# Optimization experiments

Measured on AMD Instinct MI355X. Metric: run time of the kernel, lower is better.

Reference implementation:

```python
import jax, jax.numpy as jnp
import numpy as np

NODES = 14      # input_size: nodes per graph
IN_F = 24       # seq_len: node feature dim
HID1 = 32
HID2 = 64       # hid_feats
HEADS = 2
OUT = 24        # output_size
B = 2048        # number of graphs
SLOPE = 0.2


def _make_edges():
    # fully connected (no self loops) within each 14-node graph
    pairs = np.array([(i, j) for i in range(NODES) for j in range(NODES) if i != j]).T  # [2,182]
    offs = (np.arange(B) * NODES)[:, None]
    src = (pairs[0][None, :] + offs).reshape(-1)
    dst = (pairs[1][None, :] + offs).reshape(-1)
    return np.stack([src, dst]).astype(np.int32)  # [2, 372736]


def setup_inputs() -> dict:
    key = jax.random.key(0)
    ks = jax.random.split(key, 16)
    N = B * NODES
    x = jax.random.normal(ks[0], (N, IN_F), dtype=jnp.float32)
    y = jax.random.normal(ks[1], (N, OUT), dtype=jnp.float32)
    edge_index = jnp.asarray(_make_edges())
    batch = jnp.repeat(jnp.arange(B, dtype=jnp.int32), NODES)
    s = 0.1
    params = dict(
        W1=jax.random.normal(ks[2], (IN_F, HEADS * HID1), dtype=jnp.float32) * s,
        a_src1=jax.random.normal(ks[3], (HEADS, HID1), dtype=jnp.float32) * s,
        a_dst1=jax.random.normal(ks[4], (HEADS, HID1), dtype=jnp.float32) * s,
        b1=jnp.zeros((HID1,), dtype=jnp.float32),
        W2=jax.random.normal(ks[5], (HID1, HEADS * HID2), dtype=jnp.float32) * s,
        a_src2=jax.random.normal(ks[6], (HEADS, HID2), dtype=jnp.float32) * s,
        a_dst2=jax.random.normal(ks[7], (HEADS, HID2), dtype=jnp.float32) * s,
        b2=jnp.zeros((HID2,), dtype=jnp.float32),
        Wf1=jax.random.normal(ks[8], (NODES, HID2, 8), dtype=jnp.float32) * s,
        bf1=jnp.zeros((NODES, 8), dtype=jnp.float32),
        Wf2=jax.random.normal(ks[9], (NODES, 8, OUT), dtype=jnp.float32) * s,
        bf2=jnp.zeros((NODES, OUT), dtype=jnp.float32),
    )
    return {"x": x, "y": y, "edge_index": edge_index, "batch": batch, **params}


def gat_conv(x, src, dst, W, a_src, a_dst, b):
    # PyG GATConv, concat=False (mean over heads), self-loops already in src/dst
    N = x.shape[0]
    H, F = a_src.shape
    xh = (x @ W).reshape(N, H, F)                       # [N,H,F]
    al_s = (xh * a_src).sum(-1)                         # [N,H]
    al_d = (xh * a_dst).sum(-1)                         # [N,H]
    alpha = jax.nn.leaky_relu(al_s[src] + al_d[dst], SLOPE)  # [E,H]
    amax = jax.ops.segment_max(alpha, dst, num_segments=N)
    ex = jnp.exp(alpha - amax[dst])
    den = jax.ops.segment_sum(ex, dst, num_segments=N)
    w = ex / den[dst]                                   # softmax per target node
    out = jax.ops.segment_sum(w[:, :, None] * xh[src], dst, num_segments=N)  # [N,H,F]
    return out.mean(axis=1) + b


def reference(x, y, edge_index, batch, W1, a_src1, a_dst1, b1, W2, a_src2, a_dst2, b2, Wf1, bf1, Wf2, bf2):
    N = x.shape[0]
    loops = jnp.arange(N, dtype=edge_index.dtype)
    src = jnp.concatenate([edge_index[0], loops])
    dst = jnp.concatenate([edge_index[1], loops])
    h = jax.nn.elu(gat_conv(x, src, dst, W1, a_src1, a_dst1, b1))   # [N,32]
    h = gat_conv(h, src, dst, W2, a_src2, a_dst2, b2)               # [N,64]
    # batch regroup: batch ids are contiguous per graph, so the Python
    # gather-loop in the original is exactly a reshape
    nb = N // NODES
    xg = h.reshape(nb, NODES, HID2).transpose(1, 0, 2)   # [14, B, 64]
    yg = y.reshape(nb, NODES, OUT)                       # [B, 14, out]
    # per-node-index MLP ensemble, batched over the 14 indices
    hh = jax.nn.relu(jnp.einsum('kbh,kho->kbo', xg, Wf1) + bf1[:, None, :])
    pred = jax.nn.sigmoid(jnp.einsum('kbo,kop->kbp', hh, Wf2) + bf2[:, None, :])  # [14,B,out]
    return pred, yg
```

## Files before the change

kernel.cpp:

```cpp
#include <hip/hip_runtime.h>

#define NODES 14
#define IN_F 24
#define HID1 32
#define HID2 64
#define OUT_F 24
#define SLOPE 0.2f

#define U_US1 0
#define U_UD1 48
#define U_US2 96
#define U_UD2 160

#define GPB 4
#define PHASE_FENCE() __builtin_amdgcn_sched_barrier(0)

__global__ __launch_bounds__(256) void compute_uvecs(
    const float* __restrict__ W1, const float* __restrict__ a_src1,
    const float* __restrict__ a_dst1,
    const float* __restrict__ W2, const float* __restrict__ a_src2,
    const float* __restrict__ a_dst2, float* __restrict__ u)
{
  const int tid = threadIdx.x;
  if (tid < 96) {
    const int sd = (tid >= 48), r = tid - sd * 48;
    const int h = (r >= IN_F), k = r - h * IN_F;
    const float* av = sd ? a_dst1 : a_src1;
    float s = 0.f;
#pragma unroll
    for (int f = 0; f < HID1; ++f)
      s += W1[k * 64 + h * HID1 + f] * av[h * HID1 + f];
    u[(sd ? U_UD1 : U_US1) + h * IN_F + k] = s;
  } else if (tid < 224) {
    const int j = tid - 96;
    const int sd = (j >= 64), r = j - sd * 64;
    const int h = (r >= HID1), k = r - h * HID1;
    const float* av = sd ? a_dst2 : a_src2;
    float s = 0.f;
#pragma unroll
    for (int f = 0; f < HID2; ++f)
      s += W2[k * 128 + h * HID2 + f] * av[h * HID2 + f];
    u[(sd ? U_UD2 : U_US2) + h * HID1 + k] = s;
  }
}

__global__ __launch_bounds__(64 * GPB) void gnn_fused(
    const float* __restrict__ x, const float* __restrict__ y,
    const float* __restrict__ W1, const float* __restrict__ b1,
    const float* __restrict__ W2, const float* __restrict__ b2,
    const float* __restrict__ Wf1, const float* __restrict__ bf1,
    const float* __restrict__ Wf2, const float* __restrict__ bf2,
    const float* __restrict__ uvec,
    float* __restrict__ out, int ngraphs)
{
  const int tid  = threadIdx.x;
  const int lane = tid & 63;
  const int wv   = tid >> 6;
  const int gu   = __builtin_amdgcn_readfirstlane(blockIdx.x * GPB + wv);
  if (gu >= ngraphs) return;

  __shared__ __align__(16) float h1s[GPB][NODES * 32];
  __shared__ __align__(16) float h2s[GPB][NODES * 64];
  __shared__ __align__(16) float wt[GPB][28 * 16];
  __shared__ __align__(16) float als[GPB][32];
  __shared__ __align__(16) float ald[GPB][32];
  __shared__ __align__(16) float hhs[GPB][112];

  const float* xg = x + (size_t)gu * (NODES * IN_F);

  {
    const float4* y4 = (const float4*)(y + (size_t)gu * (NODES * OUT_F));
    float4* o4 = (float4*)(out + (size_t)NODES * ngraphs * OUT_F
                               + (size_t)gu * (NODES * OUT_F));
    for (int i = lane; i < (NODES * OUT_F) / 4; i += 64) o4[i] = y4[i];
  }

  float xcol[NODES];
  {
    float w1r[IN_F];
#pragma unroll
    for (int k = 0; k < IN_F; ++k) w1r[k] = W1[k * 64 + lane];
#pragma unroll 2
    for (int n = 0; n < NODES; ++n) {
      float acc = 0.f;
#pragma unroll
      for (int k = 0; k < IN_F; ++k) acc += xg[n * IN_F + k] * w1r[k];
      xcol[n] = acc;
    }
  }
  PHASE_FENCE();

  if (lane < 56) {
    const int n = lane >> 2, h = (lane >> 1) & 1, sd = lane & 1;
    const float* uu = uvec + (sd ? U_UD1 : U_US1) + h * IN_F;
    float s = 0.f;
#pragma unroll
    for (int k4 = 0; k4 < 6; ++k4) {
      const float4 xv = *(const float4*)&xg[n * IN_F + k4 * 4];
      const float4 uv = *(const float4*)&uu[k4 * 4];
      s += xv.x * uv.x + xv.y * uv.y + xv.z * uv.z + xv.w * uv.w;
    }
    (sd ? ald : als)[wv][h * 16 + n] = s;
  }
  if (lane < NODES * 2) {
    const int j = lane >> 1, h = lane & 1;
    const float ad = ald[wv][h * 16 + j];
    const float4 A0 = *(const float4*)&als[wv][h * 16 + 0];
    const float4 A1 = *(const float4*)&als[wv][h * 16 + 4];
    const float4 A2 = *(const float4*)&als[wv][h * 16 + 8];
    const float2 A3 = *(const float2*)&als[wv][h * 16 + 12];
    float a[NODES] = {A0.x, A0.y, A0.z, A0.w, A1.x, A1.y, A1.z, A1.w,
                      A2.x, A2.y, A2.z, A2.w, A3.x, A3.y};
    float m = -1e30f;
#pragma unroll
    for (int i = 0; i < NODES; ++i) {
      float v = a[i] + ad;
      v = v > 0.f ? v : SLOPE * v;
      a[i] = v; m = fmaxf(m, v);
    }
    float den = 0.f;
#pragma unroll
    for (int i = 0; i < NODES; ++i) { a[i] = __expf(a[i] - m); den += a[i]; }
    const float r = 1.f / den;
    float* wr = &wt[wv][(j * 2 + h) * 16];
    *(float4*)&wr[0]  = make_float4(a[0]*r,  a[1]*r,  a[2]*r,  a[3]*r);
    *(float4*)&wr[4]  = make_float4(a[4]*r,  a[5]*r,  a[6]*r,  a[7]*r);
    *(float4*)&wr[8]  = make_float4(a[8]*r,  a[9]*r,  a[10]*r, a[11]*r);
    *(float2*)&wr[12] = make_float2(a[12]*r, a[13]*r);
  }
  PHASE_FENCE();

  {
    const int h = lane >> 5, f5 = lane & 31;
    const float bb = b1[f5];
#pragma unroll 2
    for (int n = 0; n < NODES; ++n) {
      const float* wr = &wt[wv][(n * 2 + h) * 16];
      const float4 w0 = *(const float4*)&wr[0];
      const float4 w1 = *(const float4*)&wr[4];
      const float4 w2 = *(const float4*)&wr[8];
      const float2 w3 = *(const float2*)&wr[12];
      float o = w0.x*xcol[0] + w0.y*xcol[1] + w0.z*xcol[2] + w0.w*xcol[3]
              + w1.x*xcol[4] + w1.y*xcol[5] + w1.z*xcol[6] + w1.w*xcol[7]
              + w2.x*xcol[8] + w2.y*xcol[9] + w2.z*xcol[10] + w2.w*xcol[11]
              + w3.x*xcol[12] + w3.y*xcol[13];
      const float oo = __shfl_xor(o, 32);
      if (h == 0) {
        const float v = 0.5f * (o + oo) + bb;
        h1s[wv][n * 32 + f5] = v > 0.f ? v : expm1f(v);
      }
    }
  }
  PHASE_FENCE();

  float acc0[NODES], acc1[NODES];
#pragma unroll
  for (int n = 0; n < NODES; ++n) { acc0[n] = 0.f; acc1[n] = 0.f; }
#pragma unroll
  for (int c = 0; c < 2; ++c) {
    float w2a[16], w2b[16];
#pragma unroll
    for (int j = 0; j < 16; ++j) {
      w2a[j] = W2[(c * 16 + j) * 128 + lane];
      w2b[j] = W2[(c * 16 + j) * 128 + 64 + lane];
    }
#pragma unroll 2
    for (int n = 0; n < NODES; ++n) {
      const float4 v0 = *(const float4*)&h1s[wv][n * 32 + c * 16 + 0];
      const float4 v1 = *(const float4*)&h1s[wv][n * 32 + c * 16 + 4];
      const float4 v2 = *(const float4*)&h1s[wv][n * 32 + c * 16 + 8];
      const float4 v3 = *(const float4*)&h1s[wv][n * 32 + c * 16 + 12];
      acc0[n] += v0.x*w2a[0] + v0.y*w2a[1] + v0.z*w2a[2] + v0.w*w2a[3]
               + v1.x*w2a[4] + v1.y*w2a[5] + v1.z*w2a[6] + v1.w*w2a[7]
               + v2.x*w2a[8] + v2.y*w2a[9] + v2.z*w2a[10] + v2.w*w2a[11]
               + v3.x*w2a[12] + v3.y*w2a[13] + v3.z*w2a[14] + v3.w*w2a[15];
      acc1[n] += v0.x*w2b[0] + v0.y*w2b[1] + v0.z*w2b[2] + v0.w*w2b[3]
               + v1.x*w2b[4] + v1.y*w2b[5] + v1.z*w2b[6] + v1.w*w2b[7]
               + v2.x*w2b[8] + v2.y*w2b[9] + v2.z*w2b[10] + v2.w*w2b[11]
               + v3.x*w2b[12] + v3.y*w2b[13] + v3.z*w2b[14] + v3.w*w2b[15];
    }
    PHASE_FENCE();
  }

  if (lane < 56) {
    const int n = lane >> 2, h = (lane >> 1) & 1, sd = lane & 1;
    const float* uu = uvec + (sd ? U_UD2 : U_US2) + h * HID1;
    float s = 0.f;
#pragma unroll
    for (int k4 = 0; k4 < 8; ++k4) {
      const float4 hv = *(const float4*)&h1s[wv][n * 32 + k4 * 4];
      const float4 uv = *(const float4*)&uu[k4 * 4];
      s += hv.x * uv.x + hv.y * uv.y + hv.z * uv.z + hv.w * uv.w;
    }
    (sd ? ald : als)[wv][h * 16 + n] = s;
  }
  if (lane < NODES * 2) {
    const int j = lane >> 1, h = lane & 1;
    const float ad = ald[wv][h * 16 + j];
    const float4 A0 = *(const float4*)&als[wv][h * 16 + 0];
    const float4 A1 = *(const float4*)&als[wv][h * 16 + 4];
    const float4 A2 = *(const float4*)&als[wv][h * 16 + 8];
    const float2 A3 = *(const float2*)&als[wv][h * 16 + 12];
    float a[NODES] = {A0.x, A0.y, A0.z, A0.w, A1.x, A1.y, A1.z, A1.w,
                      A2.x, A2.y, A2.z, A2.w, A3.x, A3.y};
    float m = -1e30f;
#pragma unroll
    for (int i = 0; i < NODES; ++i) {
      float v = a[i] + ad;
      v = v > 0.f ? v : SLOPE * v;
      a[i] = v; m = fmaxf(m, v);
    }
    float den = 0.f;
#pragma unroll
    for (int i = 0; i < NODES; ++i) { a[i] = __expf(a[i] - m); den += a[i]; }
    const float r = 1.f / den;
    float* wr = &wt[wv][(j * 2 + h) * 16];
    *(float4*)&wr[0]  = make_float4(a[0]*r,  a[1]*r,  a[2]*r,  a[3]*r);
    *(float4*)&wr[4]  = make_float4(a[4]*r,  a[5]*r,  a[6]*r,  a[7]*r);
    *(float4*)&wr[8]  = make_float4(a[8]*r,  a[9]*r,  a[10]*r, a[11]*r);
    *(float2*)&wr[12] = make_float2(a[12]*r, a[13]*r);
  }
  PHASE_FENCE();

  {
    const float bb = b2[lane];
#pragma unroll 2
    for (int n = 0; n < NODES; ++n) {
      const float* wr0 = &wt[wv][(n * 2 + 0) * 16];
      const float* wr1 = &wt[wv][(n * 2 + 1) * 16];
      const float4 p0 = *(const float4*)&wr0[0];
      const float4 p1 = *(const float4*)&wr0[4];
      const float4 p2 = *(const float4*)&wr0[8];
      const float2 p3 = *(const float2*)&wr0[12];
      const float4 q0 = *(const float4*)&wr1[0];
      const float4 q1 = *(const float4*)&wr1[4];
      const float4 q2 = *(const float4*)&wr1[8];
      const float2 q3 = *(const float2*)&wr1[12];
      const float o0 = p0.x*acc0[0] + p0.y*acc0[1] + p0.z*acc0[2] + p0.w*acc0[3]
                     + p1.x*acc0[4] + p1.y*acc0[5] + p1.z*acc0[6] + p1.w*acc0[7]
                     + p2.x*acc0[8] + p2.y*acc0[9] + p2.z*acc0[10] + p2.w*acc0[11]
                     + p3.x*acc0[12] + p3.y*acc0[13];
      const float o1 = q0.x*acc1[0] + q0.y*acc1[1] + q0.z*acc1[2] + q0.w*acc1[3]
                     + q1.x*acc1[4] + q1.y*acc1[5] + q1.z*acc1[6] + q1.w*acc1[7]
                     + q2.x*acc1[8] + q2.y*acc1[9] + q2.z*acc1[10] + q2.w*acc1[11]
                     + q3.x*acc1[12] + q3.y*acc1[13];
      h2s[wv][n * 64 + lane] = 0.5f * (o0 + o1) + bb;
    }
  }
  PHASE_FENCE();

  for (int idx = lane; idx < NODES * 8; idx += 64) {
    const int k = idx >> 3, e = idx & 7;
    float acc = bf1[k * 8 + e];
#pragma unroll
    for (int f4 = 0; f4 < 16; ++f4) {
      const float4 hv = *(const float4*)&h2s[wv][k * 64 + f4 * 4];
      acc += hv.x * Wf1[(k * HID2 + f4 * 4 + 0) * 8 + e]
           + hv.y * Wf1[(k * HID2 + f4 * 4 + 1) * 8 + e]
           + hv.z * Wf1[(k * HID2 + f4 * 4 + 2) * 8 + e]
           + hv.w * Wf1[(k * HID2 + f4 * 4 + 3) * 8 + e];
    }
    hhs[wv][idx] = fmaxf(acc, 0.f);
  }
  PHASE_FENCE();

  for (int idx = lane; idx < NODES * OUT_F; idx += 64) {
    const int k = idx / OUT_F, o = idx - k * OUT_F;
    const float4 h0 = *(const float4*)&hhs[wv][k * 8];
    const float4 h1 = *(const float4*)&hhs[wv][k * 8 + 4];
    float acc = bf2[k * OUT_F + o]
              + h0.x * Wf2[(k * 8 + 0) * OUT_F + o]
              + h0.y * Wf2[(k * 8 + 1) * OUT_F + o]
              + h0.z * Wf2[(k * 8 + 2) * OUT_F + o]
              + h0.w * Wf2[(k * 8 + 3) * OUT_F + o]
              + h1.x * Wf2[(k * 8 + 4) * OUT_F + o]
              + h1.y * Wf2[(k * 8 + 5) * OUT_F + o]
              + h1.z * Wf2[(k * 8 + 6) * OUT_F + o]
              + h1.w * Wf2[(k * 8 + 7) * OUT_F + o];
    out[(size_t)k * ngraphs * OUT_F + (size_t)gu * OUT_F + o] =
        1.f / (1.f + __expf(-acc));
  }
}

extern "C" void kernel_launch(void* const* d_in, const int* in_sizes, int n_in,
                              void* d_out, int out_size, void* d_ws, size_t ws_size,
                              hipStream_t stream) {
  const float* x      = (const float*)d_in[0];
  const float* y      = (const float*)d_in[1];
  const float* W1     = (const float*)d_in[4];
  const float* a_src1 = (const float*)d_in[5];
  const float* a_dst1 = (const float*)d_in[6];
  const float* b1     = (const float*)d_in[7];
  const float* W2     = (const float*)d_in[8];
  const float* a_src2 = (const float*)d_in[9];
  const float* a_dst2 = (const float*)d_in[10];
  const float* b2     = (const float*)d_in[11];
  const float* Wf1    = (const float*)d_in[12];
  const float* bf1    = (const float*)d_in[13];
  const float* Wf2    = (const float*)d_in[14];
  const float* bf2    = (const float*)d_in[15];
  float* out = (float*)d_out;
  float* u   = (float*)d_ws;

  const int nnodes  = in_sizes[0] / IN_F;
  const int ngraphs = nnodes / NODES;
  const int nblocks = (ngraphs + GPB - 1) / GPB;

  hipLaunchKernelGGL(compute_uvecs, dim3(1), dim3(256), 0, stream,
                     W1, a_src1, a_dst1, W2, a_src2, a_dst2, u);
  hipLaunchKernelGGL(gnn_fused, dim3(nblocks), dim3(64 * GPB), 0, stream,
                     x, y, W1, b1, W2, b2, Wf1, bf1, Wf2, bf2, u, out, ngraphs);
}
```

Before: 33.25 us.

## Pad LDS row strides, hoist W1/W2 register loads, drop phase fences

Pads the shared-memory row strides of h1s, h2s and the attention weight table (36/68/20 instead of 32/64/16) so row accesses in later phases hit different LDS banks. W1 and all 64 W2 columns are loaded into registers once at kernel start, so the global-load latency overlaps the y copy and first phase, and the W2 GEMM runs in one pass instead of two chunks. Several sched_barrier fences are removed to give the compiler more freedom to interleave phases. Holding 64 more live floats per lane raises register pressure and may lower occupancy or cause spills.

```diff
diff --git a/kernel.cpp b/kernel.cpp
--- a/kernel.cpp
+++ b/kernel.cpp
@@ -13,6 +13,9 @@
 #define U_UD2 160
 
 #define GPB 4
+#define H1_S 36
+#define H2_S 68
+#define WT_S 20
 #define PHASE_FENCE() __builtin_amdgcn_sched_barrier(0)
 
 __global__ __launch_bounds__(256) void compute_uvecs(
@@ -59,14 +62,25 @@
   const int gu   = __builtin_amdgcn_readfirstlane(blockIdx.x * GPB + wv);
   if (gu >= ngraphs) return;
 
-  __shared__ __align__(16) float h1s[GPB][NODES * 32];
-  __shared__ __align__(16) float h2s[GPB][NODES * 64];
-  __shared__ __align__(16) float wt[GPB][28 * 16];
+  __shared__ __align__(16) float h1s[GPB][NODES * H1_S];
+  __shared__ __align__(16) float h2s[GPB][NODES * H2_S];
+  __shared__ __align__(16) float wt[GPB][28 * WT_S];
   __shared__ __align__(16) float als[GPB][32];
   __shared__ __align__(16) float ald[GPB][32];
   __shared__ __align__(16) float hhs[GPB][112];
 
   const float* xg = x + (size_t)gu * (NODES * IN_F);
+
+  float w1r[IN_F];
+#pragma unroll
+  for (int k = 0; k < IN_F; ++k) w1r[k] = W1[k * 64 + lane];
+  float w2r[64];
+#pragma unroll
+  for (int k = 0; k < HID1; ++k) {
+    w2r[k]      = W2[k * 128 + lane];
+    w2r[32 + k] = W2[k * 128 + 64 + lane];
+  }
+  PHASE_FENCE();
 
   {
     const float4* y4 = (const float4*)(y + (size_t)gu * (NODES * OUT_F));
@@ -76,19 +90,13 @@
   }
 
   float xcol[NODES];
-  {
-    float w1r[IN_F];
-#pragma unroll
-    for (int k = 0; k < IN_F; ++k) w1r[k] = W1[k * 64 + lane];
 #pragma unroll 2
-    for (int n = 0; n < NODES; ++n) {
-      float acc = 0.f;
-#pragma unroll
-      for (int k = 0; k < IN_F; ++k) acc += xg[n * IN_F + k] * w1r[k];
-      xcol[n] = acc;
-    }
-  }
-  PHASE_FENCE();
+  for (int n = 0; n < NODES; ++n) {
+    float acc = 0.f;
+#pragma unroll
+    for (int k = 0; k < IN_F; ++k) acc += xg[n * IN_F + k] * w1r[k];
+    xcol[n] = acc;
+  }
 
   if (lane < 56) {
     const int n = lane >> 2, h = (lane >> 1) & 1, sd = lane & 1;
@@ -122,20 +130,19 @@
 #pragma unroll
     for (int i = 0; i < NODES; ++i) { a[i] = __expf(a[i] - m); den += a[i]; }
     const float r = 1.f / den;
-    float* wr = &wt[wv][(j * 2 + h) * 16];
+    float* wr = &wt[wv][(j * 2 + h) * WT_S];
     *(float4*)&wr[0]  = make_float4(a[0]*r,  a[1]*r,  a[2]*r,  a[3]*r);
     *(float4*)&wr[4]  = make_float4(a[4]*r,  a[5]*r,  a[6]*r,  a[7]*r);
     *(float4*)&wr[8]  = make_float4(a[8]*r,  a[9]*r,  a[10]*r, a[11]*r);
     *(float2*)&wr[12] = make_float2(a[12]*r, a[13]*r);
   }
-  PHASE_FENCE();
 
   {
     const int h = lane >> 5, f5 = lane & 31;
     const float bb = b1[f5];
 #pragma unroll 2
     for (int n = 0; n < NODES; ++n) {
-      const float* wr = &wt[wv][(n * 2 + h) * 16];
+      const float* wr = &wt[wv][(n * 2 + h) * WT_S];
       const float4 w0 = *(const float4*)&wr[0];
       const float4 w1 = *(const float4*)&wr[4];
       const float4 w2 = *(const float4*)&wr[8];
@@ -147,39 +154,39 @@
       const float oo = __shfl_xor(o, 32);
       if (h == 0) {
         const float v = 0.5f * (o + oo) + bb;
-        h1s[wv][n * 32 + f5] = v > 0.f ? v : expm1f(v);
+        h1s[wv][n * H1_S + f5] = v > 0.f ? v : expm1f(v);
       }
     }
   }
   PHASE_FENCE();
 
   float acc0[NODES], acc1[NODES];
-#pragma unroll
-  for (int n = 0; n < NODES; ++n) { acc0[n] = 0.f; acc1[n] = 0.f; }
-#pragma unroll
-  for (int c = 0; c < 2; ++c) {
-    float w2a[16], w2b[16];
-#pragma unroll
-    for (int j = 0; j < 16; ++j) {
-      w2a[j] = W2[(c * 16 + j) * 128 + lane];
-      w2b[j] = W2[(c * 16 + j) * 128 + 64 + lane];
-    }
 #pragma unroll 2
-    for (int n = 0; n < NODES; ++n) {
-      const float4 v0 = *(const float4*)&h1s[wv][n * 32 + c * 16 + 0];
-      const float4 v1 = *(const float4*)&h1s[wv][n * 32 + c * 16 + 4];
-      const float4 v2 = *(const float4*)&h1s[wv][n * 32 + c * 16 + 8];
-      const float4 v3 = *(const float4*)&h1s[wv][n * 32 + c * 16 + 12];
-      acc0[n] += v0.x*w2a[0] + v0.y*w2a[1] + v0.z*w2a[2] + v0.w*w2a[3]
-               + v1.x*w2a[4] + v1.y*w2a[5] + v1.z*w2a[6] + v1.w*w2a[7]
-               + v2.x*w2a[8] + v2.y*w2a[9] + v2.z*w2a[10] + v2.w*w2a[11]
-               + v3.x*w2a[12] + v3.y*w2a[13] + v3.z*w2a[14] + v3.w*w2a[15];
-      acc1[n] += v0.x*w2b[0] + v0.y*w2b[1] + v0.z*w2b[2] + v0.w*w2b[3]
-               + v1.x*w2b[4] + v1.y*w2b[5] + v1.z*w2b[6] + v1.w*w2b[7]
-               + v2.x*w2b[8] + v2.y*w2b[9] + v2.z*w2b[10] + v2.w*w2b[11]
-               + v3.x*w2b[12] + v3.y*w2b[13] + v3.z*w2b[14] + v3.w*w2b[15];
-    }
-    PHASE_FENCE();
+  for (int n = 0; n < NODES; ++n) {
+    const float4 v0 = *(const float4*)&h1s[wv][n * H1_S + 0];
+    const float4 v1 = *(const float4*)&h1s[wv][n * H1_S + 4];
+    const float4 v2 = *(const float4*)&h1s[wv][n * H1_S + 8];
+    const float4 v3 = *(const float4*)&h1s[wv][n * H1_S + 12];
+    const float4 v4 = *(const float4*)&h1s[wv][n * H1_S + 16];
+    const float4 v5 = *(const float4*)&h1s[wv][n * H1_S + 20];
+    const float4 v6 = *(const float4*)&h1s[wv][n * H1_S + 24];
+    const float4 v7 = *(const float4*)&h1s[wv][n * H1_S + 28];
+    acc0[n] = v0.x*w2r[0] + v0.y*w2r[1] + v0.z*w2r[2] + v0.w*w2r[3]
+            + v1.x*w2r[4] + v1.y*w2r[5] + v1.z*w2r[6] + v1.w*w2r[7]
+            + v2.x*w2r[8] + v2.y*w2r[9] + v2.z*w2r[10] + v2.w*w2r[11]
+            + v3.x*w2r[12] + v3.y*w2r[13] + v3.z*w2r[14] + v3.w*w2r[15]
+            + v4.x*w2r[16] + v4.y*w2r[17] + v4.z*w2r[18] + v4.w*w2r[19]
+            + v5.x*w2r[20] + v5.y*w2r[21] + v5.z*w2r[22] + v5.w*w2r[23]
+            + v6.x*w2r[24] + v6.y*w2r[25] + v6.z*w2r[26] + v6.w*w2r[27]
+            + v7.x*w2r[28] + v7.y*w2r[29] + v7.z*w2r[30] + v7.w*w2r[31];
+    acc1[n] = v0.x*w2r[32] + v0.y*w2r[33] + v0.z*w2r[34] + v0.w*w2r[35]
+            + v1.x*w2r[36] + v1.y*w2r[37] + v1.z*w2r[38] + v1.w*w2r[39]
+            + v2.x*w2r[40] + v2.y*w2r[41] + v2.z*w2r[42] + v2.w*w2r[43]
+            + v3.x*w2r[44] + v3.y*w2r[45] + v3.z*w2r[46] + v3.w*w2r[47]
+            + v4.x*w2r[48] + v4.y*w2r[49] + v4.z*w2r[50] + v4.w*w2r[51]
+            + v5.x*w2r[52] + v5.y*w2r[53] + v5.z*w2r[54] + v5.w*w2r[55]
+            + v6.x*w2r[56] + v6.y*w2r[57] + v6.z*w2r[58] + v6.w*w2r[59]
+            + v7.x*w2r[60] + v7.y*w2r[61] + v7.z*w2r[62] + v7.w*w2r[63];
   }
 
   if (lane < 56) {
@@ -188,7 +195,7 @@
     float s = 0.f;
 #pragma unroll
     for (int k4 = 0; k4 < 8; ++k4) {
-      const float4 hv = *(const float4*)&h1s[wv][n * 32 + k4 * 4];
+      const float4 hv = *(const float4*)&h1s[wv][n * H1_S + k4 * 4];
       const float4 uv = *(const float4*)&uu[k4 * 4];
       s += hv.x * uv.x + hv.y * uv.y + hv.z * uv.z + hv.w * uv.w;
     }
@@ -214,20 +221,19 @@
 #pragma unroll
     for (int i = 0; i < NODES; ++i) { a[i] = __expf(a[i] - m); den += a[i]; }
     const float r = 1.f / den;
-    float* wr = &wt[wv][(j * 2 + h) * 16];
+    float* wr = &wt[wv][(j * 2 + h) * WT_S];
     *(float4*)&wr[0]  = make_float4(a[0]*r,  a[1]*r,  a[2]*r,  a[3]*r);
     *(float4*)&wr[4]  = make_float4(a[4]*r,  a[5]*r,  a[6]*r,  a[7]*r);
     *(float4*)&wr[8]  = make_float4(a[8]*r,  a[9]*r,  a[10]*r, a[11]*r);
     *(float2*)&wr[12] = make_float2(a[12]*r, a[13]*r);
   }
-  PHASE_FENCE();
 
   {
     const float bb = b2[lane];
 #pragma unroll 2
     for (int n = 0; n < NODES; ++n) {
-      const float* wr0 = &wt[wv][(n * 2 + 0) * 16];
-      const float* wr1 = &wt[wv][(n * 2 + 1) * 16];
+      const float* wr0 = &wt[wv][(n * 2 + 0) * WT_S];
+      const float* wr1 = &wt[wv][(n * 2 + 1) * WT_S];
       const float4 p0 = *(const float4*)&wr0[0];
       const float4 p1 = *(const float4*)&wr0[4];
       const float4 p2 = *(const float4*)&wr0[8];
@@ -244,7 +250,7 @@
                      + q1.x*acc1[4] + q1.y*acc1[5] + q1.z*acc1[6] + q1.w*acc1[7]
                      + q2.x*acc1[8] + q2.y*acc1[9] + q2.z*acc1[10] + q2.w*acc1[11]
                      + q3.x*acc1[12] + q3.y*acc1[13];
-      h2s[wv][n * 64 + lane] = 0.5f * (o0 + o1) + bb;
+      h2s[wv][n * H2_S + lane] = 0.5f * (o0 + o1) + bb;
     }
   }
   PHASE_FENCE();
@@ -254,7 +260,7 @@
     float acc = bf1[k * 8 + e];
 #pragma unroll
     for (int f4 = 0; f4 < 16; ++f4) {
-      const float4 hv = *(const float4*)&h2s[wv][k * 64 + f4 * 4];
+      const float4 hv = *(const float4*)&h2s[wv][k * H2_S + f4 * 4];
       acc += hv.x * Wf1[(k * HID2 + f4 * 4 + 0) * 8 + e]
            + hv.y * Wf1[(k * HID2 + f4 * 4 + 1) * 8 + e]
            + hv.z * Wf1[(k * HID2 + f4 * 4 + 2) * 8 + e]
@@ -262,7 +268,6 @@
     }
     hhs[wv][idx] = fmaxf(acc, 0.f);
   }
-  PHASE_FENCE();
 
   for (int idx = lane; idx < NODES * OUT_F; idx += 64) {
     const int k = idx / OUT_F, o = idx - k * OUT_F;
```

Result: faster. 30.52 us (-8.2%).
